# Kernel optimization log

Hardware: AMD Instinct MI355X
Metric: run time of the kernel (lower is better)

## Reference

```python
import jax, jax.numpy as jnp
import numpy as np

D_MODEL = 1024
NUM_HEADS = 16
D_K = D_MODEL // NUM_HEADS
B, S = 2, 2048


def setup_inputs() -> dict:
    key = jax.random.key(0)
    ks = jax.random.split(key, 12)
    s = 1.0 / np.sqrt(D_MODEL)
    return {
        "query": jax.random.normal(ks[0], (B, S, D_MODEL), jnp.float32),
        "key": jax.random.normal(ks[1], (B, S, D_MODEL), jnp.float32),
        "value": jax.random.normal(ks[2], (B, S, D_MODEL), jnp.float32),
        "mask": jnp.ones((B, S), jnp.int32),
        "Wq": jax.random.uniform(ks[3], (D_MODEL, D_MODEL), jnp.float32, -s, s),
        "bq": jax.random.uniform(ks[4], (D_MODEL,), jnp.float32, -s, s),
        "Wk": jax.random.uniform(ks[5], (D_MODEL, D_MODEL), jnp.float32, -s, s),
        "bk": jax.random.uniform(ks[6], (D_MODEL,), jnp.float32, -s, s),
        "Wv": jax.random.uniform(ks[7], (D_MODEL, D_MODEL), jnp.float32, -s, s),
        "bv": jax.random.uniform(ks[8], (D_MODEL,), jnp.float32, -s, s),
        "Wo": jax.random.uniform(ks[9], (D_MODEL, D_MODEL), jnp.float32, -s, s),
        "bo": jax.random.uniform(ks[10], (D_MODEL,), jnp.float32, -s, s),
    }


def reference(query, key, value, mask, Wq, bq, Wk, bk, Wv, bv, Wo, bo):
    b, s, _ = query.shape
    scale = jnp.sqrt(jnp.asarray(D_K, jnp.float32)).astype(query.dtype)
    # QKV projections: x @ W.T + b (torch nn.Linear convention)
    Q = (query @ Wq.T + bq).reshape(b, s, NUM_HEADS, D_K).transpose(0, 2, 1, 3)
    K = (key @ Wk.T + bk).reshape(b, -1, NUM_HEADS, D_K).transpose(0, 2, 1, 3)
    V = (value @ Wv.T + bv).reshape(b, -1, NUM_HEADS, D_K).transpose(0, 2, 1, 3)
    # scores in fp32, then cast back to input dtype (matches source)
    scores = jnp.einsum('bhqd,bhkd->bhqk', Q.astype(jnp.float32), K.astype(jnp.float32)) / scale
    scores = scores.astype(Q.dtype)
    # 2D mask [B,S] -> [B,1,1,S], broadcast over heads/queries
    fill = jnp.finfo(scores.dtype).min
    scores = jnp.where(mask[:, None, None, :] == 0, fill, scores)
    attn = jax.nn.softmax(scores, axis=-1)  # dropout p=0 -> identity
    context = jnp.einsum('bhqk,bhkd->bhqd', attn, V)
    context = context.transpose(0, 2, 1, 3).reshape(b, s, D_MODEL)
    return context @ Wo.T + bo
```

## Files before the change

kernel.cpp:

```cpp
#include <hip/hip_runtime.h>


typedef __bf16 bf16_8 __attribute__((ext_vector_type(8)));
typedef float  f32x4  __attribute__((ext_vector_type(4)));

#define MFMA16(a, b, c) __builtin_amdgcn_mfma_f32_16x16x32_bf16((a), (b), (c), 0, 0, 0)

__device__ __forceinline__ void async_ld16(const void* g, void* l) {
  __builtin_amdgcn_global_load_lds(
      (__attribute__((address_space(1))) void*)g,
      (__attribute__((address_space(3))) void*)l, 16, 0, 0);
}

__device__ __forceinline__ void gemm_core_128(
    const __bf16* __restrict__ A, const __bf16* __restrict__ BT, int K,
    int tm, int tn, __bf16* At, __bf16* Bt, f32x4 acc[4][4]) {
  const int tid  = threadIdx.x;
  const int lane = tid & 63;
  const int w    = tid >> 6;
  const int quad = lane >> 4;
  const int c16  = lane & 15;
  const int wm = w >> 1, wn = w & 1;

  const int ch0  = w * 2;
  const int row0 = ch0 * 16 + (lane >> 2);
  const int col0 = (lane & 3) * 8;
  const __bf16* Ag = A  + (size_t)(tm + row0) * K + col0;
  const __bf16* Bg = BT + (size_t)(tn + row0) * K + col0;
  __bf16* Al = At + ch0 * 512;
  __bf16* Bl = Bt + ch0 * 512;
  const size_t rowK16 = (size_t)16 * K;

  for (int kt = 0; kt < K; kt += 32) {
    async_ld16(Ag + kt,          Al);
    async_ld16(Ag + rowK16 + kt, Al + 512);
    async_ld16(Bg + kt,          Bl);
    async_ld16(Bg + rowK16 + kt, Bl + 512);
    __syncthreads();

    bf16_8 af[4], bfr[4];
#pragma unroll
    for (int mi = 0; mi < 4; ++mi)
      af[mi] = *(const bf16_8*)(At + (wm * 64 + mi * 16 + c16) * 32 + quad * 8);
#pragma unroll
    for (int ni = 0; ni < 4; ++ni)
      bfr[ni] = *(const bf16_8*)(Bt + (wn * 64 + ni * 16 + c16) * 32 + quad * 8);
#pragma unroll
    for (int mi = 0; mi < 4; ++mi)
#pragma unroll
      for (int ni = 0; ni < 4; ++ni)
        acc[mi][ni] = MFMA16(af[mi], bfr[ni], acc[mi][ni]);
    __syncthreads();
  }
}

__global__ __launch_bounds__(256)
void qkv_fused(const __bf16* __restrict__ xq, const __bf16* __restrict__ xk,
               const __bf16* __restrict__ xv,
               const __bf16* __restrict__ wq, const __bf16* __restrict__ wk,
               const __bf16* __restrict__ wv,
               const float* __restrict__ bq, const float* __restrict__ bk,
               const float* __restrict__ bv,
               __bf16* __restrict__ Qo, __bf16* __restrict__ Ko,
               __bf16* __restrict__ Vo) {
  __shared__ __bf16 At[128 * 32];
  __shared__ __bf16 Bt[128 * 32];
  const int z  = blockIdx.z;
  const int bx = blockIdx.x;
  const __bf16 *A, *BT;
  const float* bias;
  int tm, tn;
  if (z == 2) {
    A = wv; BT = xv; bias = bv;
    tm = (bx >> 5) * 128; tn = (bx & 31) * 128;
  } else if (z == 1) {
    A = xk; BT = wk; bias = bk;
    tm = (bx >> 3) * 128; tn = (bx & 7) * 128;
  } else {
    A = xq; BT = wq; bias = bq;
    tm = (bx >> 3) * 128; tn = (bx & 7) * 128;
  }

  f32x4 acc[4][4];
  const f32x4 zero4 = {0.f, 0.f, 0.f, 0.f};
#pragma unroll
  for (int i = 0; i < 4; ++i)
#pragma unroll
    for (int j = 0; j < 4; ++j) acc[i][j] = zero4;

  gemm_core_128(A, BT, 1024, tm, tn, At, Bt, acc);

  const int lane = threadIdx.x & 63;
  const int w    = threadIdx.x >> 6;
  const int quad = lane >> 4, c16 = lane & 15;
  const int wm = w >> 1, wn = w & 1;

  if (z == 2) {
#pragma unroll
    for (int mi = 0; mi < 4; ++mi) {
#pragma unroll
      for (int ni = 0; ni < 4; ++ni) {
        const int n  = tn + wn * 64 + ni * 16 + c16;
        const int bb = n >> 11, s = n & 2047;
#pragma unroll
        for (int r = 0; r < 4; ++r) {
          const int m  = tm + wm * 64 + mi * 16 + quad * 4 + r;
          const int hh = m >> 6, d = m & 63;
          Vo[(((size_t)(bb * 16 + hh) * 64 + d) << 11) + s] =
              (__bf16)(acc[mi][ni][r] + bias[m]);
        }
      }
    }
  } else {
    __bf16* Out = (z == 1) ? Ko : Qo;
    const float scale = (z == 0) ? 0.125f : 1.0f;
#pragma unroll
    for (int mi = 0; mi < 4; ++mi) {
#pragma unroll
      for (int ni = 0; ni < 4; ++ni) {
        const int n  = tn + wn * 64 + ni * 16 + c16;
        const int hh = n >> 6, d = n & 63;
        const float bn = bias[n];
#pragma unroll
        for (int r = 0; r < 4; ++r) {
          const int m  = tm + wm * 64 + mi * 16 + quad * 4 + r;
          const int bb = m >> 11, s = m & 2047;
          Out[(((size_t)(bb * 16 + hh) * 2048 + s) << 6) + d] =
              (__bf16)((acc[mi][ni][r] + bn) * scale);
        }
      }
    }
  }
}

__global__ __launch_bounds__(256)
void out_proj(const __bf16* __restrict__ ctx, const __bf16* __restrict__ wo,
              const float* __restrict__ bo, float* __restrict__ out) {
  __shared__ __bf16 At[64 * 32];
  __shared__ __bf16 Bt[128 * 32];
  const int bx = blockIdx.x;
  const int tm = (bx >> 3) * 64, tn = (bx & 7) * 128;

  const int tid  = threadIdx.x;
  const int lane = tid & 63, w = tid >> 6;
  const int quad = lane >> 4, c16 = lane & 15;
  const int wm = w >> 1, wn = w & 1;

  const int row0 = lane >> 2, col0 = (lane & 3) * 8;
  const __bf16* Ag = ctx + (size_t)(tm + w * 16 + row0) * 1024 + col0;
  const __bf16* Bg = wo  + (size_t)(tn + w * 32 + row0) * 1024 + col0;
  __bf16* Al = At + w * 512;
  __bf16* Bl = Bt + w * 1024;

  f32x4 acc[2][4];
  const f32x4 zero4 = {0.f, 0.f, 0.f, 0.f};
#pragma unroll
  for (int i = 0; i < 2; ++i)
#pragma unroll
    for (int j = 0; j < 4; ++j) acc[i][j] = zero4;

  for (int kt = 0; kt < 1024; kt += 32) {
    async_ld16(Ag + kt, Al);
    async_ld16(Bg + kt, Bl);
    async_ld16(Bg + 16 * 1024 + kt, Bl + 512);
    __syncthreads();

    bf16_8 af[2], bfr[4];
#pragma unroll
    for (int mi = 0; mi < 2; ++mi)
      af[mi] = *(const bf16_8*)(At + (wm * 32 + mi * 16 + c16) * 32 + quad * 8);
#pragma unroll
    for (int ni = 0; ni < 4; ++ni)
      bfr[ni] = *(const bf16_8*)(Bt + (wn * 64 + ni * 16 + c16) * 32 + quad * 8);
#pragma unroll
    for (int mi = 0; mi < 2; ++mi)
#pragma unroll
      for (int ni = 0; ni < 4; ++ni)
        acc[mi][ni] = MFMA16(af[mi], bfr[ni], acc[mi][ni]);
    __syncthreads();
  }

#pragma unroll
  for (int mi = 0; mi < 2; ++mi) {
#pragma unroll
    for (int ni = 0; ni < 4; ++ni) {
      const int n = tn + wn * 64 + ni * 16 + c16;
      const float bn = bo[n];
#pragma unroll
      for (int r = 0; r < 4; ++r) {
        const int m = tm + wm * 32 + mi * 16 + quad * 4 + r;
        out[(size_t)m * 1024 + n] = acc[mi][ni][r] + bn;
      }
    }
  }
}

__global__ __launch_bounds__(256)
void flash_attn(const __bf16* __restrict__ Qg, const __bf16* __restrict__ Kg,
                const __bf16* __restrict__ VTg, const int* __restrict__ maskg,
                __bf16* __restrict__ ctx) {
  __shared__ __bf16 Kl[64 * 72];
  __shared__ __bf16 Vl[64 * 72];
  __shared__ __bf16 Pl[128 * 72];
  __shared__ float  maskadd[64];

  const int t    = threadIdx.x;
  const int lane = t & 63, w = t >> 6;
  const int quad = lane >> 4, c16 = lane & 15;
  const int qt = blockIdx.x, h = blockIdx.y, b = blockIdx.z;
  const size_t bh = (size_t)(b * 16 + h);
  const int qbase = qt * 128 + w * 32;

  bf16_8 aq[2][2];
#pragma unroll
  for (int mi = 0; mi < 2; ++mi) {
    const __bf16* qptr = Qg + (bh * 2048 + qbase + mi * 16 + c16) * 64;
    aq[mi][0] = *(const bf16_8*)(qptr + quad * 8);
    aq[mi][1] = *(const bf16_8*)(qptr + 32 + quad * 8);
  }

  f32x4 o[2][4];
  const f32x4 zero4 = {0.f, 0.f, 0.f, 0.f};
#pragma unroll
  for (int mi = 0; mi < 2; ++mi)
#pragma unroll
    for (int dt = 0; dt < 4; ++dt) o[mi][dt] = zero4;
  float lsum[2][4] = {{0.f, 0.f, 0.f, 0.f}, {0.f, 0.f, 0.f, 0.f}};

  const int srow = t >> 2;
  const int scc  = (t & 3) * 16;
  const __bf16* Kgp = Kg + bh * 2048 * 64;
  const __bf16* Vgp = VTg + bh * 64 * 2048;
  const float LOG2E = 1.44269504088896f;

  for (int kt = 0; kt < 2048; kt += 64) {
    {
      const size_t kb = (size_t)(kt + srow) * 64 + scc;
      *(bf16_8*)&Kl[srow * 72 + scc]     = *(const bf16_8*)&Kgp[kb];
      *(bf16_8*)&Kl[srow * 72 + scc + 8] = *(const bf16_8*)&Kgp[kb + 8];
      const size_t vb = (size_t)srow * 2048 + kt + scc;
      *(bf16_8*)&Vl[srow * 72 + scc]     = *(const bf16_8*)&Vgp[vb];
      *(bf16_8*)&Vl[srow * 72 + scc + 8] = *(const bf16_8*)&Vgp[vb + 8];
      if (t < 64) maskadd[t] = maskg[b * 2048 + kt + t] ? -17.3123404907f : -1e30f;
    }
    __syncthreads();

#pragma unroll
    for (int nt = 0; nt < 4; ++nt) {
      const bf16_8 b0 = *(const bf16_8*)&Kl[(nt * 16 + c16) * 72 + quad * 8];
      const bf16_8 b1 = *(const bf16_8*)&Kl[(nt * 16 + c16) * 72 + 32 + quad * 8];
      const float ma = maskadd[nt * 16 + c16];
#pragma unroll
      for (int mi = 0; mi < 2; ++mi) {
        f32x4 sf = MFMA16(aq[mi][1], b1, MFMA16(aq[mi][0], b0, zero4));
#pragma unroll
        for (int r = 0; r < 4; ++r) {
          const float p = __builtin_amdgcn_exp2f(fmaf(sf[r], LOG2E, ma));
          lsum[mi][r] += p;
          Pl[(w * 32 + mi * 16 + quad * 4 + r) * 72 + nt * 16 + c16] = (__bf16)p;
        }
      }
    }

#pragma unroll
    for (int kf = 0; kf < 2; ++kf) {
      const bf16_8 pa0 = *(const bf16_8*)&Pl[(w * 32 + c16) * 72 + kf * 32 + quad * 8];
      const bf16_8 pa1 = *(const bf16_8*)&Pl[(w * 32 + 16 + c16) * 72 + kf * 32 + quad * 8];
#pragma unroll
      for (int dt = 0; dt < 4; ++dt) {
        const bf16_8 vb = *(const bf16_8*)&Vl[(dt * 16 + c16) * 72 + kf * 32 + quad * 8];
        o[0][dt] = MFMA16(pa0, vb, o[0][dt]);
        o[1][dt] = MFMA16(pa1, vb, o[1][dt]);
      }
    }
    __syncthreads();
  }

#pragma unroll
  for (int mi = 0; mi < 2; ++mi)
#pragma unroll
    for (int r = 0; r < 4; ++r) {
      float rs = lsum[mi][r];
      rs += __shfl_xor(rs, 1);
      rs += __shfl_xor(rs, 2);
      rs += __shfl_xor(rs, 4);
      rs += __shfl_xor(rs, 8);
      lsum[mi][r] = 1.0f / rs;
    }

#pragma unroll
  for (int mi = 0; mi < 2; ++mi) {
    const int sbase = qbase + mi * 16 + quad * 4;
#pragma unroll
    for (int dt = 0; dt < 4; ++dt) {
#pragma unroll
      for (int r = 0; r < 4; ++r) {
        ctx[((size_t)b * 2048 + sbase + r) * 1024 + h * 64 + dt * 16 + c16] =
            (__bf16)(o[mi][dt][r] * lsum[mi][r]);
      }
    }
  }
}

__global__ __launch_bounds__(256)
void cvt_all(const float* __restrict__ q, const float* __restrict__ k,
             const float* __restrict__ v, const float* __restrict__ Wq,
             const float* __restrict__ Wk, const float* __restrict__ Wv,
             const float* __restrict__ Wo,
             __bf16* __restrict__ xq, __bf16* __restrict__ xk,
             __bf16* __restrict__ xv, __bf16* __restrict__ wqb,
             __bf16* __restrict__ wkb, __bf16* __restrict__ wvb,
             __bf16* __restrict__ wob) {
  const int y = blockIdx.y;
  const float* s;
  __bf16* d;
  int n8;
  switch (y) {
    case 0: s = q;  d = xq;  n8 = 524288; break;
    case 1: s = k;  d = xk;  n8 = 524288; break;
    case 2: s = v;  d = xv;  n8 = 524288; break;
    case 3: s = Wq; d = wqb; n8 = 131072; break;
    case 4: s = Wk; d = wkb; n8 = 131072; break;
    case 5: s = Wv; d = wvb; n8 = 131072; break;
    default: s = Wo; d = wob; n8 = 131072; break;
  }
  const int i = blockIdx.x * blockDim.x + threadIdx.x;
  if (i < n8) {
    const float4* sp = (const float4*)s;
    const float4 v0 = sp[i * 2], v1 = sp[i * 2 + 1];
    bf16_8 o;
    o[0] = (__bf16)v0.x; o[1] = (__bf16)v0.y;
    o[2] = (__bf16)v0.z; o[3] = (__bf16)v0.w;
    o[4] = (__bf16)v1.x; o[5] = (__bf16)v1.y;
    o[6] = (__bf16)v1.z; o[7] = (__bf16)v1.w;
    *(bf16_8*)(d + (size_t)i * 8) = o;
  }
}

extern "C" void kernel_launch(void* const* d_in, const int* in_sizes, int n_in,
                              void* d_out, int out_size, void* d_ws, size_t ws_size,
                              hipStream_t stream) {
  (void)in_sizes; (void)n_in; (void)out_size; (void)ws_size;
  const float* q    = (const float*)d_in[0];
  const float* k    = (const float*)d_in[1];
  const float* v    = (const float*)d_in[2];
  const int*   mask = (const int*)d_in[3];
  const float* Wq = (const float*)d_in[4];
  const float* bq = (const float*)d_in[5];
  const float* Wk = (const float*)d_in[6];
  const float* bk = (const float*)d_in[7];
  const float* Wv = (const float*)d_in[8];
  const float* bv = (const float*)d_in[9];
  const float* Wo = (const float*)d_in[10];
  const float* bo = (const float*)d_in[11];

  char* ws = (char*)d_ws;
  const size_t MB = 1ull << 20;
  __bf16* xq  = (__bf16*)(ws + 0 * MB);
  __bf16* xk  = (__bf16*)(ws + 8 * MB);
  __bf16* xv  = (__bf16*)(ws + 16 * MB);
  __bf16* wqb = (__bf16*)(ws + 24 * MB);
  __bf16* wkb = (__bf16*)(ws + 26 * MB);
  __bf16* wvb = (__bf16*)(ws + 28 * MB);
  __bf16* wob = (__bf16*)(ws + 30 * MB);
  __bf16* Qb  = (__bf16*)(ws + 32 * MB);
  __bf16* Kb  = (__bf16*)(ws + 40 * MB);
  __bf16* VTb = (__bf16*)(ws + 48 * MB);
  __bf16* ctx = (__bf16*)(ws + 56 * MB);

  cvt_all<<<dim3(2048, 7), 256, 0, stream>>>(q, k, v, Wq, Wk, Wv, Wo,
                                             xq, xk, xv, wqb, wkb, wvb, wob);

  qkv_fused<<<dim3(256, 1, 3), 256, 0, stream>>>(xq, xk, xv, wqb, wkb, wvb,
                                                 bq, bk, bv, Qb, Kb, VTb);

  flash_attn<<<dim3(16, 16, 2), 256, 0, stream>>>(Qb, Kb, VTb, mask, ctx);

  out_proj<<<dim3(512), 256, 0, stream>>>(ctx, wob, bo, (float*)d_out);
}
```

Before: 245.0 us.

## Rewrite flash attention with 32x32 MFMA, register-resident P and split-K halves

The attention kernel now uses 512 threads per block. The two halves of the block each process half of the key sequence and their partial outputs are merged through shared memory at the end. Scores are computed as K·Qᵀ with 32x32x16 MFMAs, and the P tile stays in registers, rearranged with v_permlane32_swap, so the LDS round trip for P is gone. Block indices are also swizzled so neighbouring blocks share a head/batch. This adds a shared-memory reduction and more LDS per block, and relies on the fixed-offset softmax staying numerically safe.

```diff
diff --git a/kernel.cpp b/kernel.cpp
--- a/kernel.cpp
+++ b/kernel.cpp
@@ -3,8 +3,11 @@
 
 typedef __bf16 bf16_8 __attribute__((ext_vector_type(8)));
 typedef float  f32x4  __attribute__((ext_vector_type(4)));
+typedef float  f32x16 __attribute__((ext_vector_type(16)));
+typedef unsigned int u32x4 __attribute__((ext_vector_type(4)));
 
 #define MFMA16(a, b, c) __builtin_amdgcn_mfma_f32_16x16x32_bf16((a), (b), (c), 0, 0, 0)
+#define MFMA32(a, b, c) __builtin_amdgcn_mfma_f32_32x32x16_bf16((a), (b), (c), 0, 0, 0)
 
 __device__ __forceinline__ void async_ld16(const void* g, void* l) {
   __builtin_amdgcn_global_load_lds(
@@ -195,109 +198,131 @@
   }
 }
 
-__global__ __launch_bounds__(256)
+__global__ __launch_bounds__(512, 4)
 void flash_attn(const __bf16* __restrict__ Qg, const __bf16* __restrict__ Kg,
                 const __bf16* __restrict__ VTg, const int* __restrict__ maskg,
                 __bf16* __restrict__ ctx) {
-  __shared__ __bf16 Kl[64 * 72];
-  __shared__ __bf16 Vl[64 * 72];
-  __shared__ __bf16 Pl[128 * 72];
-  __shared__ float  maskadd[64];
+  __shared__ __align__(16) __bf16 Kl[2][64 * 72];
+  __shared__ __align__(16) __bf16 Vl[2][64 * 72];
+  __shared__ __align__(16) float  maskadd[2][64];
+  __shared__ __align__(16) float  Om[4][32][64];
+  __shared__ float Lm[4][32];
 
   const int t    = threadIdx.x;
-  const int lane = t & 63, w = t >> 6;
-  const int quad = lane >> 4, c16 = lane & 15;
-  const int qt = blockIdx.x, h = blockIdx.y, b = blockIdx.z;
-  const size_t bh = (size_t)(b * 16 + h);
-  const int qbase = qt * 128 + w * 32;
-
-  bf16_8 aq[2][2];
-#pragma unroll
-  for (int mi = 0; mi < 2; ++mi) {
-    const __bf16* qptr = Qg + (bh * 2048 + qbase + mi * 16 + c16) * 64;
-    aq[mi][0] = *(const bf16_8*)(qptr + quad * 8);
-    aq[mi][1] = *(const bf16_8*)(qptr + 32 + quad * 8);
-  }
-
-  f32x4 o[2][4];
-  const f32x4 zero4 = {0.f, 0.f, 0.f, 0.f};
-#pragma unroll
-  for (int mi = 0; mi < 2; ++mi)
-#pragma unroll
-    for (int dt = 0; dt < 4; ++dt) o[mi][dt] = zero4;
-  float lsum[2][4] = {{0.f, 0.f, 0.f, 0.f}, {0.f, 0.f, 0.f, 0.f}};
-
-  const int srow = t >> 2;
-  const int scc  = (t & 3) * 16;
-  const __bf16* Kgp = Kg + bh * 2048 * 64;
-  const __bf16* Vgp = VTg + bh * 64 * 2048;
+  const int lane = t & 63;
+  const int w    = t >> 6;
+  const int g    = w & 3;
+  const int hh   = w >> 2;
+  const int n32  = lane & 31;
+  const int h    = lane >> 5;
+
+  const int linear = blockIdx.x + (blockIdx.y << 4) + (blockIdx.z << 8);
+  const int sw     = (linear & 7) * 64 + (linear >> 3);
+  const int qt     = sw & 15;
+  const int head   = (sw >> 4) & 15;
+  const int b      = sw >> 8;
+
+  const size_t bh = (size_t)(b * 16 + head);
+  const int qbase = qt * 128 + g * 32;
+
+  bf16_8 bq[4];
+  {
+    const __bf16* qptr = Qg + (bh * 2048 + qbase + n32) * 64 + h * 8;
+#pragma unroll
+    for (int s = 0; s < 4; ++s) bq[s] = *(const bf16_8*)(qptr + s * 16);
+  }
+
+  const f32x16 z16 = {0.f,0.f,0.f,0.f,0.f,0.f,0.f,0.f,
+                      0.f,0.f,0.f,0.f,0.f,0.f,0.f,0.f};
+  f32x16 o0 = z16, o1 = z16;
+  float lsum = 0.f;
+
+  const int tl   = t & 255;
+  const int srow = tl >> 2, scc = (tl & 3) * 16;
+  const __bf16* Kgp = Kg  + (bh * 2048 + hh * 1024) * 64;
+  const __bf16* Vgp = VTg + bh * 64 * 2048 + hh * 1024;
+  const int*    mgp = maskg + b * 2048 + hh * 1024;
   const float LOG2E = 1.44269504088896f;
 
-  for (int kt = 0; kt < 2048; kt += 64) {
+  for (int kt = 0; kt < 1024; kt += 64) {
     {
       const size_t kb = (size_t)(kt + srow) * 64 + scc;
-      *(bf16_8*)&Kl[srow * 72 + scc]     = *(const bf16_8*)&Kgp[kb];
-      *(bf16_8*)&Kl[srow * 72 + scc + 8] = *(const bf16_8*)&Kgp[kb + 8];
-      const size_t vb = (size_t)srow * 2048 + kt + scc;
-      *(bf16_8*)&Vl[srow * 72 + scc]     = *(const bf16_8*)&Vgp[vb];
-      *(bf16_8*)&Vl[srow * 72 + scc + 8] = *(const bf16_8*)&Vgp[vb + 8];
-      if (t < 64) maskadd[t] = maskg[b * 2048 + kt + t] ? -17.3123404907f : -1e30f;
-    }
-    __syncthreads();
-
-#pragma unroll
-    for (int nt = 0; nt < 4; ++nt) {
-      const bf16_8 b0 = *(const bf16_8*)&Kl[(nt * 16 + c16) * 72 + quad * 8];
-      const bf16_8 b1 = *(const bf16_8*)&Kl[(nt * 16 + c16) * 72 + 32 + quad * 8];
-      const float ma = maskadd[nt * 16 + c16];
-#pragma unroll
-      for (int mi = 0; mi < 2; ++mi) {
-        f32x4 sf = MFMA16(aq[mi][1], b1, MFMA16(aq[mi][0], b0, zero4));
-#pragma unroll
-        for (int r = 0; r < 4; ++r) {
-          const float p = __builtin_amdgcn_exp2f(fmaf(sf[r], LOG2E, ma));
-          lsum[mi][r] += p;
-          Pl[(w * 32 + mi * 16 + quad * 4 + r) * 72 + nt * 16 + c16] = (__bf16)p;
-        }
-      }
-    }
-
-#pragma unroll
-    for (int kf = 0; kf < 2; ++kf) {
-      const bf16_8 pa0 = *(const bf16_8*)&Pl[(w * 32 + c16) * 72 + kf * 32 + quad * 8];
-      const bf16_8 pa1 = *(const bf16_8*)&Pl[(w * 32 + 16 + c16) * 72 + kf * 32 + quad * 8];
-#pragma unroll
-      for (int dt = 0; dt < 4; ++dt) {
-        const bf16_8 vb = *(const bf16_8*)&Vl[(dt * 16 + c16) * 72 + kf * 32 + quad * 8];
-        o[0][dt] = MFMA16(pa0, vb, o[0][dt]);
-        o[1][dt] = MFMA16(pa1, vb, o[1][dt]);
-      }
-    }
-    __syncthreads();
-  }
-
-#pragma unroll
-  for (int mi = 0; mi < 2; ++mi)
-#pragma unroll
-    for (int r = 0; r < 4; ++r) {
-      float rs = lsum[mi][r];
-      rs += __shfl_xor(rs, 1);
-      rs += __shfl_xor(rs, 2);
-      rs += __shfl_xor(rs, 4);
-      rs += __shfl_xor(rs, 8);
-      lsum[mi][r] = 1.0f / rs;
-    }
-
-#pragma unroll
-  for (int mi = 0; mi < 2; ++mi) {
-    const int sbase = qbase + mi * 16 + quad * 4;
-#pragma unroll
-    for (int dt = 0; dt < 4; ++dt) {
-#pragma unroll
-      for (int r = 0; r < 4; ++r) {
-        ctx[((size_t)b * 2048 + sbase + r) * 1024 + h * 64 + dt * 16 + c16] =
-            (__bf16)(o[mi][dt][r] * lsum[mi][r]);
-      }
+      *(bf16_8*)&Kl[hh][srow * 72 + scc]     = *(const bf16_8*)&Kgp[kb];
+      *(bf16_8*)&Kl[hh][srow * 72 + scc + 8] = *(const bf16_8*)&Kgp[kb + 8];
+      const size_t vbi = (size_t)srow * 2048 + kt + scc;
+      *(bf16_8*)&Vl[hh][srow * 72 + scc]     = *(const bf16_8*)&Vgp[vbi];
+      *(bf16_8*)&Vl[hh][srow * 72 + scc + 8] = *(const bf16_8*)&Vgp[vbi + 8];
+      if (tl < 64) maskadd[hh][tl] = mgp[kt + tl] ? -17.3123404907f : -1e30f;
+    }
+    __syncthreads();
+
+#pragma unroll
+    for (int kt2 = 0; kt2 < 2; ++kt2) {
+      f32x16 p = z16;
+#pragma unroll
+      for (int s = 0; s < 4; ++s) {
+        const bf16_8 ka =
+            *(const bf16_8*)&Kl[hh][(kt2 * 32 + n32) * 72 + s * 16 + h * 8];
+        p = MFMA32(ka, bq[s], p);
+      }
+      unsigned c[8];
+#pragma unroll
+      for (int i = 0; i < 8; ++i) {
+        const int r0 = 2 * i, r1 = 2 * i + 1;
+        const float ma0 =
+            maskadd[hh][kt2 * 32 + (r0 & 3) + 8 * (r0 >> 2) + 4 * h];
+        const float ma1 =
+            maskadd[hh][kt2 * 32 + (r1 & 3) + 8 * (r1 >> 2) + 4 * h];
+        const float e0 = __builtin_amdgcn_exp2f(fmaf(p[r0], LOG2E, ma0));
+        const float e1 = __builtin_amdgcn_exp2f(fmaf(p[r1], LOG2E, ma1));
+        lsum += e0 + e1;
+        union { __bf16 hx[2]; unsigned u; } uu;
+        uu.hx[0] = (__bf16)e0;
+        uu.hx[1] = (__bf16)e1;
+        c[i] = uu.u;
+      }
+      asm volatile("v_permlane32_swap_b32 %0, %1" : "+v"(c[0]), "+v"(c[2]));
+      asm volatile("v_permlane32_swap_b32 %0, %1" : "+v"(c[1]), "+v"(c[3]));
+      asm volatile("v_permlane32_swap_b32 %0, %1" : "+v"(c[4]), "+v"(c[6]));
+      asm volatile("v_permlane32_swap_b32 %0, %1" : "+v"(c[5]), "+v"(c[7]));
+#pragma unroll
+      for (int sub = 0; sub < 2; ++sub) {
+        const u32x4 av = {c[4 * sub + 0], c[4 * sub + 1],
+                          c[4 * sub + 2], c[4 * sub + 3]};
+        const bf16_8 aP = __builtin_bit_cast(bf16_8, av);
+        const int s = kt2 * 2 + sub;
+        const bf16_8 vb0 =
+            *(const bf16_8*)&Vl[hh][n32 * 72 + s * 16 + h * 8];
+        const bf16_8 vb1 =
+            *(const bf16_8*)&Vl[hh][(32 + n32) * 72 + s * 16 + h * 8];
+        o0 = MFMA32(aP, vb0, o0);
+        o1 = MFMA32(aP, vb1, o1);
+      }
+    }
+    __syncthreads();
+  }
+
+  lsum += __shfl_xor(lsum, 32);
+
+  if (hh) {
+#pragma unroll
+    for (int r = 0; r < 16; ++r) {
+      const int qrow = (r & 3) + 8 * (r >> 2) + 4 * h;
+      Om[g][qrow][n32]      = o0[r];
+      Om[g][qrow][32 + n32] = o1[r];
+    }
+    if (h == 0) Lm[g][n32] = lsum;
+  }
+  __syncthreads();
+  if (!hh) {
+    const float linv = 1.0f / (lsum + Lm[g][n32]);
+#pragma unroll
+    for (int r = 0; r < 16; ++r) {
+      const int qrow = (r & 3) + 8 * (r >> 2) + 4 * h;
+      const float li = __shfl(linv, qrow);
+      __bf16* cp = ctx + ((size_t)b * 2048 + qbase + qrow) * 1024 + head * 64;
+      cp[n32]      = (__bf16)((o0[r] + Om[g][qrow][n32]) * li);
+      cp[32 + n32] = (__bf16)((o1[r] + Om[g][qrow][32 + n32]) * li);
     }
   }
 }
@@ -374,7 +399,7 @@
   qkv_fused<<<dim3(256, 1, 3), 256, 0, stream>>>(xq, xk, xv, wqb, wkb, wvb,
                                                  bq, bk, bv, Qb, Kb, VTb);
 
-  flash_attn<<<dim3(16, 16, 2), 256, 0, stream>>>(Qb, Kb, VTb, mask, ctx);
+  flash_attn<<<dim3(16, 16, 2), 512, 0, stream>>>(Qb, Kb, VTb, mask, ctx);
 
   out_proj<<<dim3(512), 256, 0, stream>>>(ctx, wob, bo, (float*)d_out);
 }
```

After: 221.4 us. -9.6%, faster.
